# Performance work log

Measured on AMD Instinct MI355X. Metric: run time of the kernel, lower is better.

The kernel has to match this reference:

```python
import jax, jax.numpy as jnp
import numpy as np

B, S, E, H = 8, 3072, 512, 8  # batch, total seq (3 chunks of 1024), emb_size, num_heads


def setup_inputs() -> dict:
    key = jax.random.key(0)
    ks = jax.random.split(key, 9)
    sc = 0.02  # weight init scale
    return {
        "x": jax.random.normal(ks[0], (B, S, E), jnp.float32),
        "Wq": jax.random.normal(ks[1], (3, E, E), jnp.float32) * sc,
        "bq": jax.random.normal(ks[2], (3, E), jnp.float32) * sc,
        "Wk": jax.random.normal(ks[3], (3, E, E), jnp.float32) * sc,
        "bk": jax.random.normal(ks[4], (3, E), jnp.float32) * sc,
        "Wv": jax.random.normal(ks[5], (3, E, E), jnp.float32) * sc,
        "bv": jax.random.normal(ks[6], (3, E), jnp.float32) * sc,
        "Wp": jax.random.normal(ks[7], (3, E, E), jnp.float32) * sc,
        "bp": jax.random.normal(ks[8], (3, E), jnp.float32) * sc,
    }


def reference(x, Wq, bq, Wk, bk, Wv, bv, Wp, bp):
    b, s, e = x.shape
    d = e // H
    # split into 3 chunks along seq: xc[c] is chunk c, shape [b, n, e]
    xc = jnp.stack(jnp.split(x, 3, axis=1))  # [3, b, n, e]

    def lin(W, bias):  # torch Linear: x @ W.T + b, per chunk
        return jnp.einsum('cbne,cfe->cbnf', xc, W) + bias[:, None, None, :]

    def heads(t):  # [3, b, n, e] -> [3, b, h, n, d]
        c, bb, n, _ = t.shape
        return t.reshape(c, bb, n, H, d).transpose(0, 1, 3, 2, 4)

    q = heads(lin(Wq, bq))
    k = heads(lin(Wk, bk))
    v = heads(lin(Wv, bv))

    # rotated cross-chunk pairing (faithful to source):
    # out1 = attn(q2, k3, v3); out2 = attn(q3, k1, v1); out3 = attn(q1, k2, v2)
    q_sel = q[jnp.array([1, 2, 0])]
    k_sel = k[jnp.array([2, 0, 1])]
    v_sel = v[jnp.array([2, 0, 1])]

    scaling = jnp.sqrt(jnp.float32(e))  # note: sqrt(emb_size), not sqrt(head_dim)
    energy = jnp.einsum('cbhqd,cbhkd->cbhqk', q_sel, k_sel) / scaling
    att = jax.nn.softmax(energy, axis=-1)  # dropout: eval-mode identity
    out = jnp.einsum('cbhqk,cbhkd->cbhqd', att, v_sel)
    out = out.transpose(0, 1, 3, 2, 4).reshape(3, b, s // 3, e)  # merge heads
    out = jnp.einsum('cbne,cfe->cbnf', out, Wp) + bp[:, None, None, :]
    return jnp.concatenate([out[0], out[1], out[2]], axis=1)  # [b, s, e]
```

## Files before the change

### kernel.cpp

```cpp
#include <hip/hip_runtime.h>
#include <hip/hip_bf16.h>


typedef __attribute__((ext_vector_type(8))) short short8v;
typedef __attribute__((ext_vector_type(4))) float float4v;
typedef __attribute__((ext_vector_type(4))) unsigned short ushort4v;
typedef __attribute__((ext_vector_type(4))) unsigned int uint4v;
typedef __attribute__((ext_vector_type(2))) unsigned int uint2v;

#define CHUNKS 3
#define BATCH 8
#define SEQ 3072
#define EMB 512
#define NH 8
#define HD 64
#define NCK 1024
#define MTOT (BATCH*SEQ)
#define QKV_ELEMS (CHUNKS*BATCH*NH*NCK*HD)
#define WELEMS (CHUNKS*EMB*EMB)
#define QSCALE 0.06375872465f

__device__ __forceinline__ unsigned short f2b(float f) {
  union { float f; unsigned int i; } x; x.f = f;
  unsigned int r = x.i + 0x7FFFu + ((x.i >> 16) & 1u);
  return (unsigned short)(r >> 16);
}
__device__ __forceinline__ unsigned int pack2r(float a, float b) {
  union { float f; unsigned int u; } xa, xb; xa.f = a; xb.f = b;
  return __builtin_amdgcn_perm(xb.u + 0x8000u, xa.u + 0x8000u, 0x07060302u);
}
__device__ __forceinline__ void gld_lds16(const unsigned short* g, unsigned short* l) {
  __builtin_amdgcn_global_load_lds(
      (const __attribute__((address_space(1))) unsigned int*)g,
      (__attribute__((address_space(3))) unsigned int*)l, 16, 0, 0);
}
#define MFMA(a, b, c) __builtin_amdgcn_mfma_f32_16x16x32_bf16(a, b, c, 0, 0, 0)

__global__ __launch_bounds__(256) void conv_x(
    const float* __restrict__ src, unsigned short* __restrict__ dst)
{
  size_t i = ((size_t)blockIdx.x * 256 + threadIdx.x) * 8;
  float4 a = *(const float4*)&src[i];
  float4 b = *(const float4*)&src[i + 4];
  uint4v p;
  p[0] = pack2r(a.x, a.y); p[1] = pack2r(a.z, a.w);
  p[2] = pack2r(b.x, b.y); p[3] = pack2r(b.z, b.w);
  *(uint4v*)&dst[i] = p;
}

__global__ __launch_bounds__(256) void conv_w(
    const float* __restrict__ s0, const float* __restrict__ s1,
    const float* __restrict__ s2, const float* __restrict__ s3,
    unsigned short* __restrict__ dst)
{
  const int z = blockIdx.y;
  const float* s = (z == 0) ? s0 : (z == 1) ? s1 : (z == 2) ? s2 : s3;
  size_t i = ((size_t)blockIdx.x * 256 + threadIdx.x) * 8;
  float4 a = *(const float4*)&s[i];
  float4 b = *(const float4*)&s[i + 4];
  uint4v p;
  p[0] = pack2r(a.x, a.y); p[1] = pack2r(a.z, a.w);
  p[2] = pack2r(b.x, b.y); p[3] = pack2r(b.z, b.w);
  *(uint4v*)&dst[(size_t)z * WELEMS + i] = p;
}

__global__ __launch_bounds__(256) void qkv_gemm(
    const unsigned short* __restrict__ xb, const unsigned short* __restrict__ Wb,
    const float* __restrict__ bq, const float* __restrict__ bk,
    const float* __restrict__ bv,
    unsigned short* __restrict__ qt, unsigned short* __restrict__ kt,
    unsigned short* __restrict__ vt)
{
  const int tid = threadIdx.x;
  const int w = tid >> 6, l = tid & 63;
  const int ln = l & 15, qu = l >> 4;
  const int sr = l >> 3, kbl = l & 7;
  const int row0 = blockIdx.x * 128;
  const int col0 = blockIdx.y * 128;
  const int z = blockIdx.z;
  const int bglob = row0 / SEQ;
  const int c = (row0 % SEQ) / NCK;
  const int n0 = row0 % NCK;
  const unsigned short* W = Wb + (size_t)z * WELEMS + c * EMB * EMB;
  const float* bias = (z == 0 ? bq : (z == 1 ? bk : bv)) + c * EMB;
  const float oscale = (z == 0) ? QSCALE : 1.0f;

  __shared__ unsigned short As[128 * 64];
  __shared__ unsigned short Bs[128 * 64];

  const int xo = (w & 1) * 64, fo = (w >> 1) * 64;

  float4v acc[4][4];
#pragma unroll
  for (int i = 0; i < 4; ++i)
#pragma unroll
    for (int j = 0; j < 4; ++j) acc[i][j] = (float4v){0.f, 0.f, 0.f, 0.f};

  for (int k0 = 0; k0 < EMB; k0 += 64) {
    __syncthreads();
#pragma unroll
    for (int s = 0; s < 4; ++s) {
      int rbase = w * 32 + s * 8;
      int r = rbase + sr;
      int kb_g = kbl ^ sr;
      gld_lds16(&xb[(size_t)(row0 + r) * EMB + k0 + kb_g * 8], &As[rbase * 64]);
      gld_lds16(&W [(size_t)(col0 + r) * EMB + k0 + kb_g * 8], &Bs[rbase * 64]);
    }
    __syncthreads();
#pragma unroll
    for (int ks = 0; ks < 2; ++ks) {
      short8v xf[4], wf[4];
#pragma unroll
      for (int i = 0; i < 4; ++i) {
        int rx = xo + 16 * i + ln;
        xf[i] = *(const short8v*)&As[rx * 64 + (((ks * 4 + qu) ^ (rx & 7)) * 8)];
        int rw = fo + 16 * i + ln;
        wf[i] = *(const short8v*)&Bs[rw * 64 + (((ks * 4 + qu) ^ (rw & 7)) * 8)];
      }
      if (z <= 1) {
#pragma unroll
        for (int i = 0; i < 4; ++i)
#pragma unroll
          for (int j = 0; j < 4; ++j) acc[i][j] = MFMA(wf[j], xf[i], acc[i][j]);
      } else {
#pragma unroll
        for (int i = 0; i < 4; ++i)
#pragma unroll
          for (int j = 0; j < 4; ++j) acc[i][j] = MFMA(xf[i], wf[j], acc[i][j]);
      }
    }
  }

  if (z <= 1) {
    unsigned short* outp = (z == 0) ? qt : kt;
#pragma unroll
    for (int j = 0; j < 4; ++j) {
      int f0 = col0 + fo + 16 * j + 4 * qu;
      float4 b4 = *(const float4*)&bias[f0];
      int hh = f0 >> 6, dd0 = f0 & 63;
      size_t base = ((size_t)((c * 8 + bglob) * 8 + hh)) << 16;
#pragma unroll
      for (int i = 0; i < 4; ++i) {
        int n = n0 + xo + 16 * i + ln;
        ushort4v p;
#pragma unroll
        for (int r = 0; r < 4; ++r)
          p[r] = f2b((acc[i][j][r] + ((const float*)&b4)[r]) * oscale);
        *(ushort4v*)&outp[base + (size_t)n * 64 + dd0] = p;
      }
    }
  } else {
#pragma unroll
    for (int i = 0; i < 4; ++i) {
      int nn0 = n0 + xo + 16 * i + 4 * qu;
#pragma unroll
      for (int j = 0; j < 4; ++j) {
        int f = col0 + fo + 16 * j + ln;
        int hh = f >> 6, dd = f & 63;
        float bvv = bias[f];
        size_t base = ((size_t)((c * 8 + bglob) * 8 + hh)) << 16;
        ushort4v p;
#pragma unroll
        for (int r = 0; r < 4; ++r) p[r] = f2b(acc[i][j][r] + bvv);
        *(ushort4v*)&vt[base + (size_t)dd * 1024 + nn0] = p;
      }
    }
  }
}

__global__ __launch_bounds__(512) void attn_kernel(
    const unsigned short* __restrict__ qt,
    const unsigned short* __restrict__ kt,
    const unsigned short* __restrict__ vt,
    unsigned short* __restrict__ attnb)
{
  const int tid = threadIdx.x;
  const int w = tid >> 6, l = tid & 63;
  const int ln = l & 15, qu = l >> 4;
  const int sr = l >> 3, kbl = l & 7;
  const int bid = blockIdx.x;
  const int hd = bid % 192;
  const int q0 = (bid / 192) * 256;
  const int co = hd >> 6;
  const int b  = (hd >> 3) & 7;
  const int h  = hd & 7;
  const int cq = (co + 1) % 3, ckv = (co + 2) % 3;
  const unsigned short* Qg = qt + ((size_t)((cq  * 8 + b) * 8 + h) << 16);
  const unsigned short* Kg = kt + ((size_t)((ckv * 8 + b) * 8 + h) << 16);
  const unsigned short* Vg = vt + ((size_t)((ckv * 8 + b) * 8 + h) << 16);

  __shared__ unsigned short Ks[64 * 64];
  __shared__ unsigned short Vs[64 * 64];
  __shared__ unsigned short Ps[8][32 * 36];

  short8v qf[2][2];
#pragma unroll
  for (int nt = 0; nt < 2; ++nt)
#pragma unroll
    for (int ks = 0; ks < 2; ++ks)
      qf[nt][ks] = *(const short8v*)&Qg[(size_t)(q0 + w * 32 + nt * 16 + ln) * 64 + ks * 32 + qu * 8];

  short8v onesf;
#pragma unroll
  for (int i = 0; i < 8; ++i) onesf[i] = (short)0x3F80;

  float4v acc_o[4][2];
#pragma unroll
  for (int i = 0; i < 4; ++i)
#pragma unroll
    for (int j = 0; j < 2; ++j) acc_o[i][j] = (float4v){0.f, 0.f, 0.f, 0.f};
  float4v acc_l[2];
  acc_l[0] = (float4v){0.f, 0.f, 0.f, 0.f};
  acc_l[1] = (float4v){0.f, 0.f, 0.f, 0.f};

  for (int kt0 = 0; kt0 < NCK; kt0 += 64) {
    __syncthreads();
    {
      int r = w * 8;
      gld_lds16(&Kg[(size_t)(kt0 + r + sr) * 64 + ((kbl ^ sr) * 8)], &Ks[r * 64]);
      gld_lds16(&Vg[(size_t)(r + sr) * 1024 + kt0 + ((kbl ^ sr) * 8)], &Vs[r * 64]);
    }
    __syncthreads();

    float4v sacc[4][2];
#pragma unroll
    for (int mt = 0; mt < 4; ++mt)
#pragma unroll
      for (int nt = 0; nt < 2; ++nt) sacc[mt][nt] = (float4v){0.f, 0.f, 0.f, 0.f};
#pragma unroll
    for (int ks = 0; ks < 2; ++ks) {
#pragma unroll
      for (int mt = 0; mt < 4; ++mt) {
        int key = 16 * mt + ln;
        short8v kf = *(const short8v*)&Ks[key * 64 + (((ks * 4 + qu) ^ (key & 7)) * 8)];
#pragma unroll
        for (int nt = 0; nt < 2; ++nt)
          sacc[mt][nt] = MFMA(kf, qf[nt][ks], sacc[mt][nt]);
      }
    }

#pragma unroll
    for (int ks2 = 0; ks2 < 2; ++ks2) {
#pragma unroll
      for (int mh = 0; mh < 2; ++mh) {
        int mt = 2 * ks2 + mh;
#pragma unroll
        for (int nt = 0; nt < 2; ++nt) {
          float e0 = __builtin_amdgcn_exp2f(sacc[mt][nt][0]);
          float e1 = __builtin_amdgcn_exp2f(sacc[mt][nt][1]);
          float e2 = __builtin_amdgcn_exp2f(sacc[mt][nt][2]);
          float e3 = __builtin_amdgcn_exp2f(sacc[mt][nt][3]);
          uint2v u;
          u[0] = pack2r(e0, e1);
          u[1] = pack2r(e2, e3);
          *(uint2v*)&Ps[w][(nt * 16 + ln) * 36 + 16 * mh + 4 * qu] = u;
        }
      }
      short8v pf[2];
#pragma unroll
      for (int nt = 0; nt < 2; ++nt)
        pf[nt] = *(const short8v*)&Ps[w][(nt * 16 + ln) * 36 + qu * 8];
#pragma unroll
      for (int nt = 0; nt < 2; ++nt)
        acc_l[nt] = MFMA(onesf, pf[nt], acc_l[nt]);
#pragma unroll
      for (int mt2 = 0; mt2 < 4; ++mt2) {
        int dd = 16 * mt2 + ln;
        short8v vf = *(const short8v*)&Vs[dd * 64 + (((ks2 * 4 + qu) ^ (dd & 7)) * 8)];
#pragma unroll
        for (int nt = 0; nt < 2; ++nt)
          acc_o[mt2][nt] = MFMA(vf, pf[nt], acc_o[mt2][nt]);
      }
    }
  }

  float inv[2];
  inv[0] = 1.0f / acc_l[0][0];
  inv[1] = 1.0f / acc_l[1][0];
  unsigned short* Og = attnb + (size_t)((co * 8 + b)) * NCK * EMB + h * HD;
#pragma unroll
  for (int mt = 0; mt < 4; ++mt) {
    int dd0 = 16 * mt + 4 * qu;
#pragma unroll
    for (int nt = 0; nt < 2; ++nt) {
      int q_glob = q0 + w * 32 + nt * 16 + ln;
      ushort4v p;
#pragma unroll
      for (int r = 0; r < 4; ++r) p[r] = f2b(acc_o[mt][nt][r] * inv[nt]);
      *(ushort4v*)&Og[(size_t)q_glob * EMB + dd0] = p;
    }
  }
}

__global__ __launch_bounds__(256) void proj_gemm(
    const unsigned short* __restrict__ attnb,
    const unsigned short* __restrict__ Wpb, const float* __restrict__ bp,
    float* __restrict__ out)
{
  const int tid = threadIdx.x;
  const int w = tid >> 6, l = tid & 63;
  const int ln = l & 15, qu = l >> 4;
  const int sr = l >> 3, kbl = l & 7;
  const int row0 = blockIdx.x * 128;
  const int col0 = blockIdx.y * 128;
  const int c = row0 >> 13;
  const int bglob = (row0 >> 10) & 7;
  const int n0 = row0 & 1023;
  const unsigned short* W = Wpb + c * EMB * EMB;
  const float* bias = bp + c * EMB;

  __shared__ unsigned short As[128 * 64];
  __shared__ unsigned short Bs[128 * 64];

  const int xo = (w & 1) * 64, fo = (w >> 1) * 64;

  float4v acc[4][4];
#pragma unroll
  for (int i = 0; i < 4; ++i)
#pragma unroll
    for (int j = 0; j < 4; ++j) acc[i][j] = (float4v){0.f, 0.f, 0.f, 0.f};

  for (int k0 = 0; k0 < EMB; k0 += 64) {
    __syncthreads();
#pragma unroll
    for (int s = 0; s < 4; ++s) {
      int rbase = w * 32 + s * 8;
      int r = rbase + sr;
      int kb_g = kbl ^ sr;
      gld_lds16(&attnb[(size_t)(row0 + r) * EMB + k0 + kb_g * 8], &As[rbase * 64]);
      gld_lds16(&W    [(size_t)(col0 + r) * EMB + k0 + kb_g * 8], &Bs[rbase * 64]);
    }
    __syncthreads();
#pragma unroll
    for (int ks = 0; ks < 2; ++ks) {
      short8v xf[4], wf[4];
#pragma unroll
      for (int i = 0; i < 4; ++i) {
        int rx = xo + 16 * i + ln;
        xf[i] = *(const short8v*)&As[rx * 64 + (((ks * 4 + qu) ^ (rx & 7)) * 8)];
        int rw = fo + 16 * i + ln;
        wf[i] = *(const short8v*)&Bs[rw * 64 + (((ks * 4 + qu) ^ (rw & 7)) * 8)];
      }
#pragma unroll
      for (int i = 0; i < 4; ++i)
#pragma unroll
        for (int j = 0; j < 4; ++j) acc[i][j] = MFMA(wf[j], xf[i], acc[i][j]);
    }
  }

#pragma unroll
  for (int j = 0; j < 4; ++j) {
    int f0 = col0 + fo + 16 * j + 4 * qu;
    float4 b4 = *(const float4*)&bias[f0];
#pragma unroll
    for (int i = 0; i < 4; ++i) {
      int srow = bglob * SEQ + c * NCK + n0 + xo + 16 * i + ln;
      float4 o;
      o.x = acc[i][j][0] + b4.x;
      o.y = acc[i][j][1] + b4.y;
      o.z = acc[i][j][2] + b4.z;
      o.w = acc[i][j][3] + b4.w;
      *(float4*)&out[(size_t)srow * EMB + f0] = o;
    }
  }
}

extern "C" void kernel_launch(void* const* d_in, const int* in_sizes, int n_in,
                              void* d_out, int out_size, void* d_ws, size_t ws_size,
                              hipStream_t stream) {
  (void)in_sizes; (void)n_in; (void)out_size; (void)ws_size;
  const float* x  = (const float*)d_in[0];
  const float* Wq = (const float*)d_in[1];
  const float* bq = (const float*)d_in[2];
  const float* Wk = (const float*)d_in[3];
  const float* bk = (const float*)d_in[4];
  const float* Wv = (const float*)d_in[5];
  const float* bv = (const float*)d_in[6];
  const float* Wp = (const float*)d_in[7];
  const float* bp = (const float*)d_in[8];
  float* out = (float*)d_out;

  unsigned short* Wb   = (unsigned short*)d_ws;
  unsigned short* qt   = Wb + 4 * (size_t)WELEMS;
  unsigned short* kt   = qt + QKV_ELEMS;
  unsigned short* vt   = kt + QKV_ELEMS;
  unsigned short* attn = vt + QKV_ELEMS;
  unsigned short* xbf  = attn;

  conv_x<<<QKV_ELEMS / (256 * 8), 256, 0, stream>>>(x, xbf);
  conv_w<<<dim3(WELEMS / (256 * 8), 4), 256, 0, stream>>>(Wq, Wk, Wv, Wp, Wb);
  qkv_gemm<<<dim3(MTOT / 128, EMB / 128, 3), 256, 0, stream>>>(
      xbf, Wb, bq, bk, bv, qt, kt, vt);
  attn_kernel<<<(NCK / 256) * CHUNKS * BATCH * NH, 512, 0, stream>>>(qt, kt, vt, attn);
  proj_gemm<<<dim3(MTOT / 128, EMB / 128), 256, 0, stream>>>(attn, Wb + 3 * (size_t)WELEMS, bp, out);
}
```

Measured before the change: 265.5 us.

## Double-buffer attention K/V tiles, widen per-wave query tile, merge conversion kernels

The attention kernel now uses 4 waves of 64 queries each instead of 8 waves of 32. K/V tiles are double-buffered in LDS, so the next tile's global-to-LDS loads overlap compute and each iteration needs one barrier instead of two. The row sum is kept in registers from the exp values and reduced with shuffles, replacing the extra ones-vector MFMA. The x and weight fp32-to-bf16 conversion kernels are merged into one launch. The trade is higher register pressure per wave and more LDS per block, which may lower occupancy.

```diff
diff --git a/kernel.cpp b/kernel.cpp
--- a/kernel.cpp
+++ b/kernel.cpp
@@ -36,32 +36,34 @@
 }
 #define MFMA(a, b, c) __builtin_amdgcn_mfma_f32_16x16x32_bf16(a, b, c, 0, 0, 0)
 
-__global__ __launch_bounds__(256) void conv_x(
-    const float* __restrict__ src, unsigned short* __restrict__ dst)
+#define XBLK (QKV_ELEMS / 2048)
+#define WBLK (WELEMS / 2048)
+__global__ __launch_bounds__(256) void conv_all(
+    const float* __restrict__ x,
+    const float* __restrict__ w0, const float* __restrict__ w1,
+    const float* __restrict__ w2, const float* __restrict__ w3,
+    unsigned short* __restrict__ xbf, unsigned short* __restrict__ Wb)
 {
-  size_t i = ((size_t)blockIdx.x * 256 + threadIdx.x) * 8;
+  const int bid = blockIdx.x;
+  const float* src;
+  unsigned short* dst;
+  size_t i;
+  if (bid < XBLK) {
+    src = x; dst = xbf;
+    i = ((size_t)bid * 256 + threadIdx.x) * 8;
+  } else {
+    const int z = (bid - XBLK) / WBLK;
+    const int ob = (bid - XBLK) % WBLK;
+    src = (z == 0) ? w0 : (z == 1) ? w1 : (z == 2) ? w2 : w3;
+    dst = Wb + (size_t)z * WELEMS;
+    i = ((size_t)ob * 256 + threadIdx.x) * 8;
+  }
   float4 a = *(const float4*)&src[i];
   float4 b = *(const float4*)&src[i + 4];
   uint4v p;
   p[0] = pack2r(a.x, a.y); p[1] = pack2r(a.z, a.w);
   p[2] = pack2r(b.x, b.y); p[3] = pack2r(b.z, b.w);
   *(uint4v*)&dst[i] = p;
-}
-
-__global__ __launch_bounds__(256) void conv_w(
-    const float* __restrict__ s0, const float* __restrict__ s1,
-    const float* __restrict__ s2, const float* __restrict__ s3,
-    unsigned short* __restrict__ dst)
-{
-  const int z = blockIdx.y;
-  const float* s = (z == 0) ? s0 : (z == 1) ? s1 : (z == 2) ? s2 : s3;
-  size_t i = ((size_t)blockIdx.x * 256 + threadIdx.x) * 8;
-  float4 a = *(const float4*)&s[i];
-  float4 b = *(const float4*)&s[i + 4];
-  uint4v p;
-  p[0] = pack2r(a.x, a.y); p[1] = pack2r(a.z, a.w);
-  p[2] = pack2r(b.x, b.y); p[3] = pack2r(b.z, b.w);
-  *(uint4v*)&dst[(size_t)z * WELEMS + i] = p;
 }
 
 __global__ __launch_bounds__(256) void qkv_gemm(
@@ -168,7 +170,7 @@
   }
 }
 
-__global__ __launch_bounds__(512) void attn_kernel(
+__global__ __launch_bounds__(256, 3) void attn_kernel(
     const unsigned short* __restrict__ qt,
     const unsigned short* __restrict__ kt,
     const unsigned short* __restrict__ vt,
@@ -189,104 +191,102 @@
   const unsigned short* Kg = kt + ((size_t)((ckv * 8 + b) * 8 + h) << 16);
   const unsigned short* Vg = vt + ((size_t)((ckv * 8 + b) * 8 + h) << 16);
 
-  __shared__ unsigned short Ks[64 * 64];
-  __shared__ unsigned short Vs[64 * 64];
-  __shared__ unsigned short Ps[8][32 * 36];
-
-  short8v qf[2][2];
-#pragma unroll
-  for (int nt = 0; nt < 2; ++nt)
+  __shared__ unsigned short Ks[2][64 * 64];
+  __shared__ unsigned short Vs[2][64 * 64];
+  __shared__ unsigned short Ps[4][64 * 36];
+
+  const float4v zero4 = {0.f, 0.f, 0.f, 0.f};
+
+  short8v qf[4][2];
+#pragma unroll
+  for (int nt = 0; nt < 4; ++nt)
 #pragma unroll
     for (int ks = 0; ks < 2; ++ks)
-      qf[nt][ks] = *(const short8v*)&Qg[(size_t)(q0 + w * 32 + nt * 16 + ln) * 64 + ks * 32 + qu * 8];
-
-  short8v onesf;
-#pragma unroll
-  for (int i = 0; i < 8; ++i) onesf[i] = (short)0x3F80;
-
-  float4v acc_o[4][2];
+      qf[nt][ks] = *(const short8v*)&Qg[(size_t)(q0 + w * 64 + nt * 16 + ln) * 64 + ks * 32 + qu * 8];
+
+  float4v acc_o[4][4];
 #pragma unroll
   for (int i = 0; i < 4; ++i)
 #pragma unroll
-    for (int j = 0; j < 2; ++j) acc_o[i][j] = (float4v){0.f, 0.f, 0.f, 0.f};
-  float4v acc_l[2];
-  acc_l[0] = (float4v){0.f, 0.f, 0.f, 0.f};
-  acc_l[1] = (float4v){0.f, 0.f, 0.f, 0.f};
-
-  for (int kt0 = 0; kt0 < NCK; kt0 += 64) {
-    __syncthreads();
-    {
-      int r = w * 8;
-      gld_lds16(&Kg[(size_t)(kt0 + r + sr) * 64 + ((kbl ^ sr) * 8)], &Ks[r * 64]);
-      gld_lds16(&Vg[(size_t)(r + sr) * 1024 + kt0 + ((kbl ^ sr) * 8)], &Vs[r * 64]);
-    }
-    __syncthreads();
-
-    float4v sacc[4][2];
-#pragma unroll
-    for (int mt = 0; mt < 4; ++mt)
-#pragma unroll
-      for (int nt = 0; nt < 2; ++nt) sacc[mt][nt] = (float4v){0.f, 0.f, 0.f, 0.f};
-#pragma unroll
-    for (int ks = 0; ks < 2; ++ks) {
-#pragma unroll
-      for (int mt = 0; mt < 4; ++mt) {
+    for (int j = 0; j < 4; ++j) acc_o[i][j] = zero4;
+  float lsum[4] = {0.f, 0.f, 0.f, 0.f};
+
+#define STAGE(buf, kt0_)                                                        \
+  {                                                                             \
+    _Pragma("unroll")                                                           \
+    for (int s = 0; s < 2; ++s) {                                               \
+      int rbase = w * 16 + s * 8;                                               \
+      int r = rbase + sr;                                                       \
+      gld_lds16(&Kg[(size_t)((kt0_) + r) * 64 + ((kbl ^ sr) * 8)],              \
+                &Ks[buf][rbase * 64]);                                          \
+      gld_lds16(&Vg[(size_t)r * 1024 + (kt0_) + ((kbl ^ sr) * 8)],              \
+                &Vs[buf][rbase * 64]);                                          \
+    }                                                                           \
+  }
+
+  STAGE(0, 0)
+  for (int t = 0; t < 16; ++t) {
+    const int cur = t & 1;
+    __syncthreads();
+    if (t < 15) STAGE(cur ^ 1, (t + 1) * 64)
+
+#pragma unroll
+    for (int half = 0; half < 2; ++half) {
+#pragma unroll
+      for (int mh = 0; mh < 2; ++mh) {
+        int mt = half * 2 + mh;
         int key = 16 * mt + ln;
-        short8v kf = *(const short8v*)&Ks[key * 64 + (((ks * 4 + qu) ^ (key & 7)) * 8)];
-#pragma unroll
-        for (int nt = 0; nt < 2; ++nt)
-          sacc[mt][nt] = MFMA(kf, qf[nt][ks], sacc[mt][nt]);
-      }
-    }
-
-#pragma unroll
-    for (int ks2 = 0; ks2 < 2; ++ks2) {
-#pragma unroll
-      for (int mh = 0; mh < 2; ++mh) {
-        int mt = 2 * ks2 + mh;
-#pragma unroll
-        for (int nt = 0; nt < 2; ++nt) {
-          float e0 = __builtin_amdgcn_exp2f(sacc[mt][nt][0]);
-          float e1 = __builtin_amdgcn_exp2f(sacc[mt][nt][1]);
-          float e2 = __builtin_amdgcn_exp2f(sacc[mt][nt][2]);
-          float e3 = __builtin_amdgcn_exp2f(sacc[mt][nt][3]);
+        short8v kf0 = *(const short8v*)&Ks[cur][key * 64 + ((qu ^ (key & 7)) * 8)];
+        short8v kf1 = *(const short8v*)&Ks[cur][key * 64 + (((4 + qu) ^ (key & 7)) * 8)];
+#pragma unroll
+        for (int nt = 0; nt < 4; ++nt) {
+          float4v s4 = MFMA(kf0, qf[nt][0], zero4);
+          s4 = MFMA(kf1, qf[nt][1], s4);
+          float e0 = __builtin_amdgcn_exp2f(s4[0]);
+          float e1 = __builtin_amdgcn_exp2f(s4[1]);
+          float e2 = __builtin_amdgcn_exp2f(s4[2]);
+          float e3 = __builtin_amdgcn_exp2f(s4[3]);
+          lsum[nt] += (e0 + e1) + (e2 + e3);
           uint2v u;
           u[0] = pack2r(e0, e1);
           u[1] = pack2r(e2, e3);
           *(uint2v*)&Ps[w][(nt * 16 + ln) * 36 + 16 * mh + 4 * qu] = u;
         }
       }
-      short8v pf[2];
-#pragma unroll
-      for (int nt = 0; nt < 2; ++nt)
+      short8v pf[4];
+#pragma unroll
+      for (int nt = 0; nt < 4; ++nt)
         pf[nt] = *(const short8v*)&Ps[w][(nt * 16 + ln) * 36 + qu * 8];
 #pragma unroll
-      for (int nt = 0; nt < 2; ++nt)
-        acc_l[nt] = MFMA(onesf, pf[nt], acc_l[nt]);
-#pragma unroll
-      for (int mt2 = 0; mt2 < 4; ++mt2) {
-        int dd = 16 * mt2 + ln;
-        short8v vf = *(const short8v*)&Vs[dd * 64 + (((ks2 * 4 + qu) ^ (dd & 7)) * 8)];
-#pragma unroll
-        for (int nt = 0; nt < 2; ++nt)
-          acc_o[mt2][nt] = MFMA(vf, pf[nt], acc_o[mt2][nt]);
-      }
-    }
-  }
-
-  float inv[2];
-  inv[0] = 1.0f / acc_l[0][0];
-  inv[1] = 1.0f / acc_l[1][0];
+      for (int mtv = 0; mtv < 4; ++mtv) {
+        int dd = 16 * mtv + ln;
+        short8v vf = *(const short8v*)&Vs[cur][dd * 64 + (((half * 4 + qu) ^ (dd & 7)) * 8)];
+#pragma unroll
+        for (int nt = 0; nt < 4; ++nt)
+          acc_o[mtv][nt] = MFMA(vf, pf[nt], acc_o[mtv][nt]);
+      }
+    }
+  }
+#undef STAGE
+
+  float inv[4];
+#pragma unroll
+  for (int nt = 0; nt < 4; ++nt) {
+    float tt = lsum[nt];
+    tt += __shfl_xor(tt, 16);
+    tt += __shfl_xor(tt, 32);
+    inv[nt] = 1.0f / tt;
+  }
   unsigned short* Og = attnb + (size_t)((co * 8 + b)) * NCK * EMB + h * HD;
 #pragma unroll
-  for (int mt = 0; mt < 4; ++mt) {
-    int dd0 = 16 * mt + 4 * qu;
-#pragma unroll
-    for (int nt = 0; nt < 2; ++nt) {
-      int q_glob = q0 + w * 32 + nt * 16 + ln;
+  for (int mtv = 0; mtv < 4; ++mtv) {
+    int dd0 = 16 * mtv + 4 * qu;
+#pragma unroll
+    for (int nt = 0; nt < 4; ++nt) {
+      int q_glob = q0 + w * 64 + nt * 16 + ln;
       ushort4v p;
 #pragma unroll
-      for (int r = 0; r < 4; ++r) p[r] = f2b(acc_o[mt][nt][r] * inv[nt]);
+      for (int r = 0; r < 4; ++r) p[r] = f2b(acc_o[mtv][nt][r] * inv[nt]);
       *(ushort4v*)&Og[(size_t)q_glob * EMB + dd0] = p;
     }
   }
@@ -387,10 +387,9 @@
   unsigned short* attn = vt + QKV_ELEMS;
   unsigned short* xbf  = attn;
 
-  conv_x<<<QKV_ELEMS / (256 * 8), 256, 0, stream>>>(x, xbf);
-  conv_w<<<dim3(WELEMS / (256 * 8), 4), 256, 0, stream>>>(Wq, Wk, Wv, Wp, Wb);
+  conv_all<<<XBLK + 4 * WBLK, 256, 0, stream>>>(x, Wq, Wk, Wv, Wp, xbf, Wb);
   qkv_gemm<<<dim3(MTOT / 128, EMB / 128, 3), 256, 0, stream>>>(
       xbf, Wb, bq, bk, bv, qt, kt, vt);
-  attn_kernel<<<(NCK / 256) * CHUNKS * BATCH * NH, 512, 0, stream>>>(qt, kt, vt, attn);
+  attn_kernel<<<(NCK / 256) * CHUNKS * BATCH * NH, 256, 0, stream>>>(qt, kt, vt, attn);
   proj_gemm<<<dim3(MTOT / 128, EMB / 128), 256, 0, stream>>>(attn, Wb + 3 * (size_t)WELEMS, bp, out);
 }
```

Measured after the change: 402.6 us. +51.7%, slower.
